# Kernel optimization log

Hardware: AMD Instinct MI355X
Metric: run time of the kernel (lower is better)

The kernel has to match this reference:

```python
import jax, jax.numpy as jnp
import numpy as np

T, H, F = 4096, 4096, 14336

def setup_inputs() -> dict:
    key = jax.random.key(0)
    k1, k2, k3, k4 = jax.random.split(key, 4)
    s = 1.0 / np.sqrt(H)
    return {
        "x": jax.random.normal(k1, (T, H), dtype=jnp.float32),
        "expert_w1": jax.random.normal(k2, (H, F), dtype=jnp.float32) * s,
        "expert_v1": jax.random.normal(k3, (H, F), dtype=jnp.float32) * s,
        "expert_w2": jax.random.normal(k4, (H, F), dtype=jnp.float32) * s,
    }

def reference(x, expert_w1, expert_v1, expert_w2):
    # SwiGLU expert FFN: silu(x @ w1) * (x @ v1) @ w2.T
    gate_proj = jax.nn.silu(x @ expert_w1)          # [T, F]
    up_proj = x @ expert_v1                          # [T, F]
    down_proj = (gate_proj * up_proj) @ expert_w2.T  # [T, H]
    return down_proj
```

## Files before the change

kernel.cpp:

```cpp
#include <hip/hip_runtime.h>
#include <hip/hip_bf16.h>
#include <stdint.h>

#define TT 4096
#define HH 4096
#define FF 14336
#define NCAT (2 * FF)

typedef __attribute__((ext_vector_type(8))) short bf16x8;
typedef __attribute__((ext_vector_type(4))) float f32x4;

__device__ __forceinline__ unsigned short f32_to_bf16(float f) {
    union { float f; unsigned int u; } v; v.f = f;
    unsigned int r = v.u + 0x7FFFu + ((v.u >> 16) & 1u);
    return (unsigned short)(r >> 16);
}

#define GLOAD16(g, l)                                                          \
    __builtin_amdgcn_global_load_lds(                                          \
        (const __attribute__((address_space(1))) void*)(g),                    \
        (__attribute__((address_space(3))) void*)(l), 16, 0, 0)

__global__ void cvt_lin(const float* __restrict__ in,
                        unsigned short* __restrict__ out, long n4) {
    long stride = (long)gridDim.x * blockDim.x;
    for (long i = (long)blockIdx.x * blockDim.x + threadIdx.x; i < n4; i += stride) {
        float4 v = *(const float4*)(in + i * 4);
        ushort4 o;
        o.x = f32_to_bf16(v.x); o.y = f32_to_bf16(v.y);
        o.z = f32_to_bf16(v.z); o.w = f32_to_bf16(v.w);
        *(ushort4*)(out + i * 4) = o;
    }
}

__global__ void cvt_tri(const float* __restrict__ in,
                        unsigned short* __restrict__ out, int off) {
    __shared__ float tile[64][65];
    int bh = blockIdx.x & 63;
    int bf = blockIdx.x >> 6;
    int t = threadIdx.x;
    int r16 = t >> 4;
    int c4 = (t & 15) * 4;
#pragma unroll
    for (int it = 0; it < 4; ++it) {
        int h = r16 + it * 16;
        float4 v = *(const float4*)(in + (size_t)(bh * 64 + h) * FF + bf * 64 + c4);
        tile[h][c4 + 0] = v.x; tile[h][c4 + 1] = v.y;
        tile[h][c4 + 2] = v.z; tile[h][c4 + 3] = v.w;
    }
    __syncthreads();
#pragma unroll
    for (int it = 0; it < 4; ++it) {
        int f = r16 + it * 16;
        int fg = bf * 64 + f;
        int row_out = ((fg >> 4) << 5) + (fg & 15) + off;
        ushort4 o;
        o.x = f32_to_bf16(tile[c4 + 0][f]);
        o.y = f32_to_bf16(tile[c4 + 1][f]);
        o.z = f32_to_bf16(tile[c4 + 2][f]);
        o.w = f32_to_bf16(tile[c4 + 3][f]);
        *(ushort4*)(out + (size_t)row_out * HH + bh * 64 + c4) = o;
    }
}


#define STG_A(BUF, SLOT, T) do {                                               \
    char* d_ = (char*)smem + (((BUF)*2 + (SLOT)) << 14) + tid * 16;            \
    GLOAD16(Abase + (size_t)(oA[SLOT][0] + (unsigned)(T) * 128), d_);          \
    GLOAD16(Abase + (size_t)(oA[SLOT][1] + (unsigned)(T) * 128), d_ + 8192);   \
  } while (0)

#define STG_B(BUF, SLOT, T) do {                                               \
    char* d_ = (char*)smem + 65536 + (((BUF)*2 + (SLOT)) << 14) + tid * 16;    \
    GLOAD16(Bbase + (size_t)(oB[SLOT][0] + (unsigned)(T) * 128), d_);          \
    GLOAD16(Bbase + (size_t)(oB[SLOT][1] + (unsigned)(T) * 128), d_ + 8192);   \
  } while (0)

#define READ_A(DST, BUF, MQ) do {                                              \
    const char* pA_ = (const char*)smem + (((BUF)*2 + (MQ)) << 14);            \
    _Pragma("unroll") for (int i_ = 0; i_ < 4; ++i_)                           \
    _Pragma("unroll") for (int k_ = 0; k_ < 2; ++k_)                           \
      DST[i_][k_] = *(const bf16x8*)(pA_ + ((((wr*64 + i_*16 + fr) << 7) + k_*64 + kg2) ^ lmask)); \
  } while (0)

#define READ_B(DST, BUF, NQ) do {                                              \
    const char* pB_ = (const char*)smem + 65536 + (((BUF)*2 + (NQ)) << 14);    \
    _Pragma("unroll") for (int j_ = 0; j_ < 2; ++j_)                           \
    _Pragma("unroll") for (int k_ = 0; k_ < 2; ++k_)                           \
      DST[j_][k_] = *(const bf16x8*)(pB_ + ((((wc*32 + j_*16 + fr) << 7) + k_*64 + kg2) ^ lmask)); \
  } while (0)

#define MFMA_Q(MQ, NQ, AF, BF)                                                 \
    _Pragma("unroll") for (int i_ = 0; i_ < 4; ++i_)                           \
    _Pragma("unroll") for (int j_ = 0; j_ < 2; ++j_)                           \
    _Pragma("unroll") for (int k_ = 0; k_ < 2; ++k_)                           \
      acc[MQ][i_][NQ][j_] = __builtin_amdgcn_mfma_f32_16x16x32_bf16(           \
          AF[i_][k_], BF[j_][k_], acc[MQ][i_][NQ][j_], 0, 0, 0)

#define BAR do {                                                               \
    asm volatile("" ::: "memory");                                             \
    __builtin_amdgcn_s_barrier();                                              \
    asm volatile("" ::: "memory");                                             \
  } while (0)

#define VMC8 asm volatile("s_waitcnt vmcnt(8)" ::: "memory")
#define VMC0 asm volatile("s_waitcnt vmcnt(0)" ::: "memory")

#define PHX(READS, STAGES, MQ, NQ, AF, BF, FENCE, POST) do {                   \
    READS;                                                                     \
    STAGES;                                                                    \
    __builtin_amdgcn_s_setprio(1);                                             \
    MFMA_Q(MQ, NQ, AF, BF);                                                    \
    __builtin_amdgcn_s_setprio(0);                                             \
    FENCE;                                                                     \
    POST;                                                                      \
    BAR;                                                                       \
  } while (0)

#define PH(READS, STAGES, MQ, NQ, AF, BF, FENCE)                               \
    PHX(READS, STAGES, MQ, NQ, AF, BF, FENCE, )

#define HALF_STG(BUF, OB, TS)                                                  \
    PH(READ_A(af, BUF, 0), , 0, 0, af, bfA, );                                 \
    PH(READ_B(bfB, BUF, 1), STG_A(BUF, 0, TS); STG_B(BUF, 0, TS), 0, 1, af, bfB, ); \
    PH(READ_A(af, BUF, 1), STG_B(BUF, 1, TS), 1, 1, af, bfB, );                \
    PHX(, STG_A(BUF, 1, TS), 1, 0, af, bfA, VMC8, READ_B(bfA, OB, 0));

#define HALF_T1(BUF, OB)                                                       \
    PH(READ_A(af, BUF, 0), , 0, 0, af, bfA, );                                 \
    PH(READ_B(bfB, BUF, 1), , 0, 1, af, bfB, );                                \
    PH(READ_A(af, BUF, 1), , 1, 1, af, bfB, );                                 \
    PHX(, , 1, 0, af, bfA, VMC0, READ_B(bfA, OB, 0));

#define HALF_T2(BUF)                                                           \
    PH(READ_A(af, BUF, 0), , 0, 0, af, bfA, );                                 \
    PH(READ_B(bfB, BUF, 1), , 0, 1, af, bfB, );                                \
    PH(READ_A(af, BUF, 1), , 1, 1, af, bfB, );                                 \
    PHX(, , 1, 0, af, bfA, , );

#define GEMM8_CORE(A_, LDA_, B_, LDB_, NT_)                                    \
  extern __shared__ char smem[];                                               \
  const char* const Abase = (const char*)(A_);                                 \
  const char* const Bbase = (const char*)(B_);                                 \
  const int tid = threadIdx.x;                                                 \
  const int lane = tid & 63;                                                   \
  const int wid = tid >> 6;                                                    \
  const int wr = wid >> 2;                                                     \
  const int wc = wid & 3;                                                      \
  const int fr = lane & 15;                                                    \
  const int kg2 = ((lane >> 4) & 3) << 4;                                      \
  const int lmask = (fr & 6) << 4;                                             \
  f32x4 acc[2][4][2][2];                                                       \
  _Pragma("unroll") for (int a_ = 0; a_ < 2; ++a_)                             \
  _Pragma("unroll") for (int b_ = 0; b_ < 4; ++b_)                             \
  _Pragma("unroll") for (int c_ = 0; c_ < 2; ++c_)                             \
  _Pragma("unroll") for (int d_ = 0; d_ < 2; ++d_)                             \
    acc[a_][b_][c_][d_] = (f32x4){0.f, 0.f, 0.f, 0.f};                         \
  bf16x8 af[4][2], bfA[2][2], bfB[2][2];                                       \
  unsigned int oA[2][2], oB[2][2];                                             \
  _Pragma("unroll") for (int c_ = 0; c_ < 2; ++c_) {                           \
    int d_ = (tid + 512 * c_) * 16;                                            \
    int p_ = d_ ^ (((d_ >> 8) & 3) << 5);                                      \
    int prow = p_ >> 7, pcol = (p_ & 127) >> 1;                                \
    _Pragma("unroll") for (int s_ = 0; s_ < 2; ++s_) {                         \
      int grA = m0 + ((prow >> 6) & 1) * 128 + s_ * 64 + (prow & 63);          \
      oA[s_][c_] = (unsigned)((size_t)grA * (LDA_) + pcol) * 2u;               \
      int grB = n0 + (prow >> 5) * 64 + s_ * 32 + (prow & 31);                 \
      oB[s_][c_] = (unsigned)((size_t)grB * (LDB_) + pcol) * 2u;               \
    }                                                                          \
  }                                                                            \
     \
  STG_A(0, 0, 0); STG_B(0, 0, 0); STG_B(0, 1, 0); STG_A(0, 1, 0);              \
  STG_A(1, 0, 1); STG_B(1, 0, 1); STG_B(1, 1, 1); STG_A(1, 1, 1);              \
  VMC8;                                                                        \
  __builtin_amdgcn_s_barrier();                                                \
  asm volatile("" ::: "memory");                                               \
  READ_B(bfA, 0, 0);                                                           \
  const int niter = (NT_) / 2;                                                 \
  for (int I = 0; I < niter - 1; ++I) {                                        \
    HALF_STG(0, 1, 2 * I + 2)                                                  \
    HALF_STG(1, 0, 2 * I + 3)                                                  \
  }                                                                            \
  HALF_T1(0, 1)                                                                \
  HALF_T2(1)

__global__ __launch_bounds__(512)
__attribute__((amdgpu_waves_per_eu(1, 2))) void gemm_swiglu(
    const unsigned short* __restrict__ Xb,
    const unsigned short* __restrict__ Wcat,
    unsigned short* __restrict__ Act) {
    const int NWG = (TT / 256) * (NCAT / 256);
    int lid = (blockIdx.x & 7) * (NWG / 8) + (blockIdx.x >> 3);
    const int m0 = (lid & 15) * 256;
    const int n0 = (lid >> 4) * 256;

    GEMM8_CORE(Xb, HH, Wcat, HH, HH / 64)

    const int dm = ((lane >> 4) & 3) * 4;
    const int dn = lane & 15;
#pragma unroll
    for (int mq = 0; mq < 2; ++mq)
#pragma unroll
        for (int i = 0; i < 4; ++i)
#pragma unroll
            for (int nq = 0; nq < 2; ++nq) {
                int rowb = m0 + wr * 128 + mq * 64 + i * 16 + dm;
                int col = (n0 + wc * 64 + nq * 32) / 2 + dn;
                f32x4 g4 = acc[mq][i][nq][0];
                f32x4 u4 = acc[mq][i][nq][1];
#pragma unroll
                for (int r = 0; r < 4; ++r) {
                    float g = g4[r], u = u4[r];
                    float s = g * u / (1.0f + __expf(-g));
                    Act[(size_t)(rowb + r) * FF + col] = f32_to_bf16(s);
                }
            }
}

__global__ __launch_bounds__(512)
__attribute__((amdgpu_waves_per_eu(1, 2))) void gemm_down(
    const unsigned short* __restrict__ Act,
    const unsigned short* __restrict__ W2b,
    float* __restrict__ Out) {
    const int NWG = (TT / 256) * (HH / 256);
    int lid = (blockIdx.x & 7) * (NWG / 8) + (blockIdx.x >> 3);
    const int m0 = (lid & 15) * 256;
    const int n0 = (lid >> 4) * 256;

    GEMM8_CORE(Act, FF, W2b, FF, FF / 64)

    const int dm = ((lane >> 4) & 3) * 4;
    const int dn = lane & 15;
#pragma unroll
    for (int mq = 0; mq < 2; ++mq)
#pragma unroll
        for (int i = 0; i < 4; ++i)
#pragma unroll
            for (int nq = 0; nq < 2; ++nq)
#pragma unroll
                for (int j = 0; j < 2; ++j) {
                    int rowb = m0 + wr * 128 + mq * 64 + i * 16 + dm;
                    int col = n0 + wc * 64 + nq * 32 + j * 16 + dn;
                    f32x4 v = acc[mq][i][nq][j];
#pragma unroll
                    for (int r = 0; r < 4; ++r)
                        Out[(size_t)(rowb + r) * HH + col] = v[r];
                }
}

extern "C" void kernel_launch(void* const* d_in, const int* in_sizes, int n_in,
                              void* d_out, int out_size, void* d_ws, size_t ws_size,
                              hipStream_t stream) {
    const float* x  = (const float*)d_in[0];
    const float* w1 = (const float*)d_in[1];
    const float* v1 = (const float*)d_in[2];
    const float* w2 = (const float*)d_in[3];
    float* out = (float*)d_out;

    unsigned short* xb   = (unsigned short*)d_ws;
    unsigned short* wcat = xb + (size_t)TT * HH;
    unsigned short* w2b  = wcat + (size_t)NCAT * HH;
    unsigned short* act  = w2b + (size_t)HH * FF;

    hipFuncSetAttribute((const void*)gemm_swiglu,
                        hipFuncAttributeMaxDynamicSharedMemorySize, 131072);
    hipFuncSetAttribute((const void*)gemm_down,
                        hipFuncAttributeMaxDynamicSharedMemorySize, 131072);

    cvt_lin<<<2048, 256, 0, stream>>>(x, xb, (long)TT * HH / 4);
    cvt_lin<<<2048, 256, 0, stream>>>(w2, w2b, (long)HH * FF / 4);
    cvt_tri<<<(HH / 64) * (FF / 64), 256, 0, stream>>>(w1, wcat, 0);
    cvt_tri<<<(HH / 64) * (FF / 64), 256, 0, stream>>>(v1, wcat, 16);

    gemm_swiglu<<<(TT / 256) * (NCAT / 256), 512, 131072, stream>>>(xb, wcat, act);
    gemm_down<<<(TT / 256) * (HH / 256), 512, 131072, stream>>>(act, w2b, out);
}
```

Measured before the change: 1.300 ms.

## Switch GEMM cores from 16x16x32 to 32x32x16 bf16 MFMA tiles

Replaces the 16x16x32 MFMA inner loop with 32x32x16 bf16 MFMA in both GEMMs. This changes the LDS fragment reads, the accumulator layout (f32x16), the staging offsets, and the epilogue row/column mapping. The gate/up interleave in the concatenated weight becomes 32-row groups so each 32-wide MFMA output holds matching gate and up columns. The aim is fewer MFMA issues and fewer LDS fragment loads per unit of work. The risk is different register pressure and possible LDS bank conflicts from the new swizzled read pattern.

```diff
diff --git a/kernel.cpp b/kernel.cpp
--- a/kernel.cpp
+++ b/kernel.cpp
@@ -9,6 +9,7 @@
 
 typedef __attribute__((ext_vector_type(8))) short bf16x8;
 typedef __attribute__((ext_vector_type(4))) float f32x4;
+typedef __attribute__((ext_vector_type(16))) float f32x16;
 
 __device__ __forceinline__ unsigned short f32_to_bf16(float f) {
     union { float f; unsigned int u; } v; v.f = f;
@@ -53,7 +54,7 @@
     for (int it = 0; it < 4; ++it) {
         int f = r16 + it * 16;
         int fg = bf * 64 + f;
-        int row_out = ((fg >> 4) << 5) + (fg & 15) + off;
+        int row_out = ((fg >> 5) << 6) + (fg & 31) + off;
         ushort4 o;
         o.x = f32_to_bf16(tile[c4 + 0][f]);
         o.y = f32_to_bf16(tile[c4 + 1][f]);
@@ -66,36 +67,36 @@
 
 #define STG_A(BUF, SLOT, T) do {                                               \
     char* d_ = (char*)smem + (((BUF)*2 + (SLOT)) << 14) + tid * 16;            \
-    GLOAD16(Abase + (size_t)(oA[SLOT][0] + (unsigned)(T) * 128), d_);          \
-    GLOAD16(Abase + (size_t)(oA[SLOT][1] + (unsigned)(T) * 128), d_ + 8192);   \
+    GLOAD16(Abase + ((size_t)oA[SLOT] + (size_t)(T) * 128), d_);               \
+    GLOAD16(Abase + ((size_t)oA[SLOT] + CA + (size_t)(T) * 128), d_ + 8192);   \
   } while (0)
 
 #define STG_B(BUF, SLOT, T) do {                                               \
     char* d_ = (char*)smem + 65536 + (((BUF)*2 + (SLOT)) << 14) + tid * 16;    \
-    GLOAD16(Bbase + (size_t)(oB[SLOT][0] + (unsigned)(T) * 128), d_);          \
-    GLOAD16(Bbase + (size_t)(oB[SLOT][1] + (unsigned)(T) * 128), d_ + 8192);   \
+    GLOAD16(Bbase + ((size_t)oB[SLOT] + (size_t)(T) * 128), d_);               \
+    GLOAD16(Bbase + ((size_t)oB[SLOT] + CB + (size_t)(T) * 128), d_ + 8192);   \
   } while (0)
 
 #define READ_A(DST, BUF, MQ) do {                                              \
     const char* pA_ = (const char*)smem + (((BUF)*2 + (MQ)) << 14);            \
-    _Pragma("unroll") for (int i_ = 0; i_ < 4; ++i_)                           \
-    _Pragma("unroll") for (int k_ = 0; k_ < 2; ++k_)                           \
-      DST[i_][k_] = *(const bf16x8*)(pA_ + ((((wr*64 + i_*16 + fr) << 7) + k_*64 + kg2) ^ lmask)); \
+    _Pragma("unroll") for (int mb_ = 0; mb_ < 2; ++mb_)                        \
+    _Pragma("unroll") for (int ks_ = 0; ks_ < 4; ++ks_)                        \
+      DST[mb_][ks_] = *(const bf16x8*)(pA_ + ((wr*64 + mb_*32 + r31) << 7)     \
+                                           + (((ks_ << 5) ^ lmask) + kh16));   \
   } while (0)
 
 #define READ_B(DST, BUF, NQ) do {                                              \
     const char* pB_ = (const char*)smem + 65536 + (((BUF)*2 + (NQ)) << 14);    \
-    _Pragma("unroll") for (int j_ = 0; j_ < 2; ++j_)                           \
-    _Pragma("unroll") for (int k_ = 0; k_ < 2; ++k_)                           \
-      DST[j_][k_] = *(const bf16x8*)(pB_ + ((((wc*32 + j_*16 + fr) << 7) + k_*64 + kg2) ^ lmask)); \
+    _Pragma("unroll") for (int ks_ = 0; ks_ < 4; ++ks_)                        \
+      DST[ks_] = *(const bf16x8*)(pB_ + ((wc*32 + r31) << 7)                   \
+                                      + (((ks_ << 5) ^ lmask) + kh16));        \
   } while (0)
 
 #define MFMA_Q(MQ, NQ, AF, BF)                                                 \
-    _Pragma("unroll") for (int i_ = 0; i_ < 4; ++i_)                           \
-    _Pragma("unroll") for (int j_ = 0; j_ < 2; ++j_)                           \
-    _Pragma("unroll") for (int k_ = 0; k_ < 2; ++k_)                           \
-      acc[MQ][i_][NQ][j_] = __builtin_amdgcn_mfma_f32_16x16x32_bf16(           \
-          AF[i_][k_], BF[j_][k_], acc[MQ][i_][NQ][j_], 0, 0, 0)
+    _Pragma("unroll") for (int ks_ = 0; ks_ < 4; ++ks_)                        \
+    _Pragma("unroll") for (int mb_ = 0; mb_ < 2; ++mb_)                        \
+      acc[MQ][mb_][NQ] = __builtin_amdgcn_mfma_f32_32x32x16_bf16(              \
+          AF[mb_][ks_], BF[ks_], acc[MQ][mb_][NQ], 0, 0, 0)
 
 #define BAR do {                                                               \
     asm volatile("" ::: "memory");                                             \
@@ -142,31 +143,33 @@
   extern __shared__ char smem[];                                               \
   const char* const Abase = (const char*)(A_);                                 \
   const char* const Bbase = (const char*)(B_);                                 \
+  const size_t CA = (size_t)(LDA_) * 256;                                      \
+  const size_t CB = (size_t)(LDB_) * 256;                                      \
   const int tid = threadIdx.x;                                                 \
   const int lane = tid & 63;                                                   \
   const int wid = tid >> 6;                                                    \
   const int wr = wid >> 2;                                                     \
   const int wc = wid & 3;                                                      \
-  const int fr = lane & 15;                                                    \
-  const int kg2 = ((lane >> 4) & 3) << 4;                                      \
-  const int lmask = (fr & 6) << 4;                                             \
-  f32x4 acc[2][4][2][2];                                                       \
+  const int r31 = lane & 31;                                                   \
+  const int kh16 = ((lane >> 5) << 4);                                         \
+  const int lmask = (lane & 6) << 4;                                           \
+  f32x16 acc[2][2][2];                                                         \
   _Pragma("unroll") for (int a_ = 0; a_ < 2; ++a_)                             \
-  _Pragma("unroll") for (int b_ = 0; b_ < 4; ++b_)                             \
+  _Pragma("unroll") for (int b_ = 0; b_ < 2; ++b_)                             \
   _Pragma("unroll") for (int c_ = 0; c_ < 2; ++c_)                             \
-  _Pragma("unroll") for (int d_ = 0; d_ < 2; ++d_)                             \
-    acc[a_][b_][c_][d_] = (f32x4){0.f, 0.f, 0.f, 0.f};                         \
-  bf16x8 af[4][2], bfA[2][2], bfB[2][2];                                       \
-  unsigned int oA[2][2], oB[2][2];                                             \
-  _Pragma("unroll") for (int c_ = 0; c_ < 2; ++c_) {                           \
-    int d_ = (tid + 512 * c_) * 16;                                            \
+  _Pragma("unroll") for (int e_ = 0; e_ < 16; ++e_)                            \
+    acc[a_][b_][c_][e_] = 0.f;                                                 \
+  bf16x8 af[2][4], bfA[4], bfB[4];                                             \
+  unsigned int oA[2], oB[2];                                                   \
+  {                                                                            \
+    int d_ = tid * 16;                                                         \
     int p_ = d_ ^ (((d_ >> 8) & 3) << 5);                                      \
     int prow = p_ >> 7, pcol = (p_ & 127) >> 1;                                \
     _Pragma("unroll") for (int s_ = 0; s_ < 2; ++s_) {                         \
-      int grA = m0 + ((prow >> 6) & 1) * 128 + s_ * 64 + (prow & 63);          \
-      oA[s_][c_] = (unsigned)((size_t)grA * (LDA_) + pcol) * 2u;               \
+      int grA = m0 + s_ * 64 + (prow & 63);                                    \
+      oA[s_] = (unsigned)((size_t)grA * (LDA_) + pcol) * 2u;                   \
       int grB = n0 + (prow >> 5) * 64 + s_ * 32 + (prow & 31);                 \
-      oB[s_][c_] = (unsigned)((size_t)grB * (LDB_) + pcol) * 2u;               \
+      oB[s_] = (unsigned)((size_t)grB * (LDB_) + pcol) * 2u;                   \
     }                                                                          \
   }                                                                            \
      \
@@ -196,25 +199,24 @@
 
     GEMM8_CORE(Xb, HH, Wcat, HH, HH / 64)
 
-    const int dm = ((lane >> 4) & 3) * 4;
-    const int dn = lane & 15;
+    const int col32 = lane & 31;
+    const int rb = (lane >> 5) * 4;
 #pragma unroll
     for (int mq = 0; mq < 2; ++mq)
 #pragma unroll
-        for (int i = 0; i < 4; ++i)
-#pragma unroll
-            for (int nq = 0; nq < 2; ++nq) {
-                int rowb = m0 + wr * 128 + mq * 64 + i * 16 + dm;
-                int col = (n0 + wc * 64 + nq * 32) / 2 + dn;
-                f32x4 g4 = acc[mq][i][nq][0];
-                f32x4 u4 = acc[mq][i][nq][1];
-#pragma unroll
-                for (int r = 0; r < 4; ++r) {
-                    float g = g4[r], u = u4[r];
-                    float s = g * u / (1.0f + __expf(-g));
-                    Act[(size_t)(rowb + r) * FF + col] = f32_to_bf16(s);
-                }
+        for (int mb = 0; mb < 2; ++mb) {
+            f32x16 g16 = acc[mq][mb][0];
+            f32x16 u16 = acc[mq][mb][1];
+            int f = (n0 >> 1) + wc * 32 + col32;
+            int row0 = m0 + wr * 128 + mq * 64 + mb * 32 + rb;
+#pragma unroll
+            for (int reg = 0; reg < 16; ++reg) {
+                int row = row0 + (reg & 3) + 8 * (reg >> 2);
+                float g = g16[reg], u = u16[reg];
+                float s = g * u / (1.0f + __expf(-g));
+                Act[(size_t)row * FF + f] = f32_to_bf16(s);
             }
+        }
 }
 
 __global__ __launch_bounds__(512)
@@ -229,23 +231,23 @@
 
     GEMM8_CORE(Act, FF, W2b, FF, FF / 64)
 
-    const int dm = ((lane >> 4) & 3) * 4;
-    const int dn = lane & 15;
+    const int col32 = lane & 31;
+    const int rb = (lane >> 5) * 4;
 #pragma unroll
     for (int mq = 0; mq < 2; ++mq)
 #pragma unroll
-        for (int i = 0; i < 4; ++i)
-#pragma unroll
-            for (int nq = 0; nq < 2; ++nq)
-#pragma unroll
-                for (int j = 0; j < 2; ++j) {
-                    int rowb = m0 + wr * 128 + mq * 64 + i * 16 + dm;
-                    int col = n0 + wc * 64 + nq * 32 + j * 16 + dn;
-                    f32x4 v = acc[mq][i][nq][j];
-#pragma unroll
-                    for (int r = 0; r < 4; ++r)
-                        Out[(size_t)(rowb + r) * HH + col] = v[r];
+        for (int mb = 0; mb < 2; ++mb)
+#pragma unroll
+            for (int nq = 0; nq < 2; ++nq) {
+                f32x16 v = acc[mq][mb][nq];
+                int col = n0 + wc * 64 + nq * 32 + col32;
+                int row0 = m0 + wr * 128 + mq * 64 + mb * 32 + rb;
+#pragma unroll
+                for (int reg = 0; reg < 16; ++reg) {
+                    int row = row0 + (reg & 3) + 8 * (reg >> 2);
+                    Out[(size_t)row * HH + col] = v[reg];
                 }
+            }
 }
 
 extern "C" void kernel_launch(void* const* d_in, const int* in_sizes, int n_in,
@@ -270,7 +272,7 @@
     cvt_lin<<<2048, 256, 0, stream>>>(x, xb, (long)TT * HH / 4);
     cvt_lin<<<2048, 256, 0, stream>>>(w2, w2b, (long)HH * FF / 4);
     cvt_tri<<<(HH / 64) * (FF / 64), 256, 0, stream>>>(w1, wcat, 0);
-    cvt_tri<<<(HH / 64) * (FF / 64), 256, 0, stream>>>(v1, wcat, 16);
+    cvt_tri<<<(HH / 64) * (FF / 64), 256, 0, stream>>>(v1, wcat, 32);
 
     gemm_swiglu<<<(TT / 256) * (NCAT / 256), 512, 131072, stream>>>(xb, wcat, act);
     gemm_down<<<(TT / 256) * (HH / 256), 512, 131072, stream>>>(act, w2b, out);
```

Result: slower. 1.441 ms (+10.9%).
